# Optimization experiments

Hardware: AMD Instinct MI355X
Metric: run time of the kernel (lower is better)

Reference implementation:

```python
import math
import jax, jax.numpy as jnp
import numpy as np

TAU = 2.0
THR = 1.0
ALPHA = 10.0

T, B, IN_DIM, OUT_DIM = 64, 128, 2048, 2048


def setup_inputs() -> dict:
    key = jax.random.key(0)
    k1, k2, k3 = jax.random.split(key, 3)
    x_seq = jax.random.normal(k1, (T, B, IN_DIM), dtype=jnp.float32)
    # scale like nn.Linear default init so membrane potentials are O(1)
    W = jax.random.normal(k2, (OUT_DIM, IN_DIM), dtype=jnp.float32) / math.sqrt(IN_DIM)
    b = jax.random.normal(k3, (OUT_DIM,), dtype=jnp.float32) * 0.01
    return {"x_seq": x_seq, "W": W, "b": b}


def spike(x):
    # forward: hard threshold (surrogate gradient only matters in bwd)
    return (x > 0).astype(x.dtype)


def reference(x_seq, W, b):
    decay = math.exp(-1.0 / TAU)
    # hoist the linear layer out of the recurrence: one big GEMM
    cur_seq = jnp.einsum("tbi,oi->tbo", x_seq, W) + b  # (T, B, OUT_DIM)
    mem0 = jnp.zeros((x_seq.shape[1], W.shape[0]), dtype=x_seq.dtype)

    def step(mem, cur):
        mem = mem * decay + cur
        spk = spike(mem - THR)
        mem = mem - spk * THR
        return mem, spk

    _, spk_seq = jax.lax.scan(step, mem0, cur_seq)
    return spk_seq  # (T, B, OUT_DIM)
```

## Files before the change

kernel.cpp:

```cpp
#include <hip/hip_runtime.h>
#include <hip/hip_bf16.h>
#include <math.h>


typedef unsigned short u16;
typedef __attribute__((ext_vector_type(8))) short bf16x8;
typedef __attribute__((ext_vector_type(4))) float f32x4;

constexpr int T_STEPS = 64;
constexpr int BATCH   = 128;
constexpr int K_DIM   = 2048;
constexpr int N_DIM   = 2048;
constexpr int M_DIM   = T_STEPS * BATCH;
constexpr int NCHAIN  = BATCH * N_DIM;

constexpr float DECAY_F32 = (float)0.6065306597126334;
constexpr float BAND      = 2e-4f;

__global__ __launch_bounds__(512, 2)
void gemm_bf16x3f(const float* __restrict__ X, const float* __restrict__ W,
                  const float* __restrict__ bias, float* __restrict__ C,
                  unsigned int* __restrict__ counters) {
    extern __shared__ __align__(16) u16 smem[];
    u16* const sAh = smem;
    u16* const sAl = smem + 2 * 8192;
    u16* const sBh = smem + 4 * 8192;
    u16* const sBl = smem + 4 * 8192 + 2 * 4096;

    const int tid  = threadIdx.x;
    const int orig = blockIdx.x + gridDim.x * blockIdx.y;
    if (orig == 0 && tid < 128) counters[tid] = 0u;

    const int wg   = (orig & 7) * 64 + (orig >> 3);
    const int m0   = (wg >> 4) * 256;
    const int n0   = (wg & 15) * 128;
    const int lane = tid & 63;
    const int wave = tid >> 6;
    const int wm   = wave >> 1;
    const int wn   = wave & 1;

    const int row_e = (tid >> 6) * 16 + (tid & 15);
    const int ks_e  = ((tid >> 4) & 3) * 8;
    const size_t a0f = (size_t)(m0 + row_e) * K_DIM + ks_e;
    const size_t a1f = (size_t)(m0 + 128 + row_e) * K_DIM + ks_e;
    const size_t b0f = (size_t)(n0 + row_e) * K_DIM + ks_e;
    const int wA0 = tid * 8;
    const int wA1 = 4096 + tid * 8;
    const int wB0 = tid * 8;

    f32x4 acc[4][4];
#pragma unroll
    for (int i = 0; i < 4; i++)
#pragma unroll
        for (int j = 0; j < 4; j++) acc[i][j] = (f32x4){0.f, 0.f, 0.f, 0.f};

    float4 g0[6], g1[6];

#define GLOAD(SET, kc) do {                                                  \
        const size_t k_ = (size_t)(kc) * 32;                                 \
        g##SET[0] = *(const float4*)(X + a0f + k_);                          \
        g##SET[1] = *(const float4*)(X + a0f + k_ + 4);                      \
        g##SET[2] = *(const float4*)(X + a1f + k_);                          \
        g##SET[3] = *(const float4*)(X + a1f + k_ + 4);                      \
        g##SET[4] = *(const float4*)(W + b0f + k_);                          \
        g##SET[5] = *(const float4*)(W + b0f + k_ + 4);                      \
    } while (0)

#define DEK8(v0, v1, HI, LO) do {                                            \
        const float f_[8] = {v0.x, v0.y, v0.z, v0.w, v1.x, v1.y, v1.z, v1.w};\
        unsigned int hp_[4], lp_[4];                                         \
        _Pragma("unroll")                                                    \
        for (int q_ = 0; q_ < 8; q_ += 2) {                                  \
            u16 hh_[2], ll_[2];                                              \
            _Pragma("unroll")                                                \
            for (int e_ = 0; e_ < 2; e_++) {                                 \
                __hip_bfloat16 hb_ = __float2bfloat16(f_[q_ + e_]);          \
                const float hf_ = __bfloat162float(hb_);                     \
                __hip_bfloat16 lb_ = __float2bfloat16(f_[q_ + e_] - hf_);    \
                hh_[e_] = *(u16*)&hb_;                                       \
                ll_[e_] = *(u16*)&lb_;                                       \
            }                                                                \
            hp_[q_ >> 1] = (unsigned int)hh_[0] | ((unsigned int)hh_[1] << 16); \
            lp_[q_ >> 1] = (unsigned int)ll_[0] | ((unsigned int)ll_[1] << 16); \
        }                                                                    \
        HI = make_uint4(hp_[0], hp_[1], hp_[2], hp_[3]);                     \
        LO = make_uint4(lp_[0], lp_[1], lp_[2], lp_[3]);                     \
    } while (0)

#define CONVWRITE(s, SET) do {                                               \
        uint4 hA0_, lA0_, hA1_, lA1_, hB_, lB_;                              \
        DEK8(g##SET[0], g##SET[1], hA0_, lA0_);                              \
        DEK8(g##SET[2], g##SET[3], hA1_, lA1_);                              \
        DEK8(g##SET[4], g##SET[5], hB_, lB_);                                \
        *(uint4*)&sAh[(s) * 8192 + wA0] = hA0_;                              \
        *(uint4*)&sAl[(s) * 8192 + wA0] = lA0_;                              \
        *(uint4*)&sAh[(s) * 8192 + wA1] = hA1_;                              \
        *(uint4*)&sAl[(s) * 8192 + wA1] = lA1_;                              \
        *(uint4*)&sBh[(s) * 4096 + wB0] = hB_;                               \
        *(uint4*)&sBl[(s) * 4096 + wB0] = lB_;                               \
    } while (0)

#define COMPUTE(rs) do {                                                     \
        bf16x8 fah[4], fal[4], fbh[4], fbl[4];                               \
        _Pragma("unroll")                                                    \
        for (int ti = 0; ti < 4; ti++) {                                     \
            const int ta = wm * 4 + ti;                                      \
            fah[ti] = *(const bf16x8*)&sAh[(rs) * 8192 + (ta * 64 + lane) * 8]; \
            fal[ti] = *(const bf16x8*)&sAl[(rs) * 8192 + (ta * 64 + lane) * 8]; \
        }                                                                    \
        _Pragma("unroll")                                                    \
        for (int tj = 0; tj < 4; tj++) {                                     \
            const int tb = wn * 4 + tj;                                      \
            fbh[tj] = *(const bf16x8*)&sBh[(rs) * 4096 + (tb * 64 + lane) * 8]; \
            fbl[tj] = *(const bf16x8*)&sBl[(rs) * 4096 + (tb * 64 + lane) * 8]; \
        }                                                                    \
        __builtin_amdgcn_s_setprio(1);                                       \
        _Pragma("unroll")                                                    \
        for (int ti = 0; ti < 4; ti++)                                       \
        _Pragma("unroll")                                                    \
        for (int tj = 0; tj < 4; tj++) {                                     \
            acc[ti][tj] = __builtin_amdgcn_mfma_f32_16x16x32_bf16(           \
                fah[ti], fbh[tj], acc[ti][tj], 0, 0, 0);                     \
            acc[ti][tj] = __builtin_amdgcn_mfma_f32_16x16x32_bf16(           \
                fah[ti], fbl[tj], acc[ti][tj], 0, 0, 0);                     \
            acc[ti][tj] = __builtin_amdgcn_mfma_f32_16x16x32_bf16(           \
                fal[ti], fbh[tj], acc[ti][tj], 0, 0, 0);                     \
        }                                                                    \
        __builtin_amdgcn_s_setprio(0);                                       \
    } while (0)

#define BAR do {                                                             \
        __builtin_amdgcn_sched_barrier(0);                                   \
        __builtin_amdgcn_s_barrier();                                        \
        __builtin_amdgcn_sched_barrier(0);                                   \
    } while (0)
#define VMW(n) do {                                                          \
        asm volatile("s_waitcnt vmcnt(" #n ")" ::: "memory");                \
        __builtin_amdgcn_sched_barrier(0);                                   \
    } while (0)
#define LGKM0 do {                                                           \
        asm volatile("s_waitcnt lgkmcnt(0)" ::: "memory");                   \
        __builtin_amdgcn_sched_barrier(0);                                   \
    } while (0)

    GLOAD(0, 0);
    VMW(0);
    CONVWRITE(0, 0);
    GLOAD(1, 1);
    LGKM0;

    for (int kc = 0; kc < 60; kc += 2) {
        BAR;
        GLOAD(0, kc + 2);
        VMW(6);
        CONVWRITE(1, 1);
        LGKM0;
        COMPUTE(0);
        BAR;
        GLOAD(1, kc + 3);
        VMW(6);
        CONVWRITE(0, 0);
        LGKM0;
        COMPUTE(1);
    }
    BAR;
    GLOAD(0, 62);
    VMW(6);
    CONVWRITE(1, 1);
    LGKM0;
    COMPUTE(0);
    BAR;
    GLOAD(1, 63);
    VMW(6);
    CONVWRITE(0, 0);
    LGKM0;
    COMPUTE(1);
    BAR;
    VMW(0);
    CONVWRITE(1, 1);
    LGKM0;
    COMPUTE(0);
    BAR;
    COMPUTE(1);

#undef LGKM0
#undef VMW
#undef BAR
#undef COMPUTE
#undef CONVWRITE
#undef DEK8
#undef GLOAD

#pragma unroll
    for (int tj = 0; tj < 4; tj++) {
        const int n  = n0 + wn * 64 + tj * 16 + (lane & 15);
        const float bv = bias[n];
#pragma unroll
        for (int ti = 0; ti < 4; ti++) {
            const int mbase = m0 + wm * 64 + ti * 16 + (lane >> 4) * 4;
#pragma unroll
            for (int r = 0; r < 4; r++)
                C[(size_t)(mbase + r) * N_DIM + n] = acc[ti][tj][r] + bv;
        }
    }
}

__global__ __launch_bounds__(256)
void lif_scan_band2(float* __restrict__ buf, unsigned int* __restrict__ counters,
                    unsigned int* __restrict__ worklist) {
    const int idx = (blockIdx.x * 256 + threadIdx.x) * 2;
    float mem[2]  = {0.f, 0.f};
    bool  flag[2] = {false, false};
#pragma unroll
    for (int t = 0; t < T_STEPS; t++) {
        const size_t off = (size_t)t * NCHAIN + idx;
        const float2 v = *(const float2*)(buf + off);
        const float c[2] = {v.x, v.y};
        float s[2];
#pragma unroll
        for (int q = 0; q < 2; q++) {
            mem[q] = __fadd_rn(__fmul_rn(mem[q], DECAY_F32), c[q]);
            const float d = __fsub_rn(mem[q], 1.0f);
            const bool spk = d > 0.0f;
            if (fabsf(d) < BAND) flag[q] = true;
            s[q] = spk ? 1.0f : 0.0f;
            if (spk) mem[q] = __fsub_rn(mem[q], 1.0f);
        }
        *(float2*)(buf + off) = make_float2(s[0], s[1]);
    }
    const int b = idx >> 11;
#pragma unroll
    for (int q = 0; q < 2; q++) {
        if (flag[q]) {
            const unsigned int p = atomicAdd(&counters[b], 1u);
            worklist[b * 2048 + p] = (unsigned int)((idx + q) & 2047);
        }
    }
}

#define RG 16
#define RJ 4
#define BKR 64

__global__ __launch_bounds__(256)
void lif_repair2(const float* __restrict__ X, const float* __restrict__ W,
                 const float* __restrict__ bias,
                 const unsigned int* __restrict__ counters,
                 const unsigned int* __restrict__ worklist,
                 float* __restrict__ out) {
    __shared__ float sX[BKR][T_STEPS + 1];
    __shared__ float sW[RG][BKR + 1];
    __shared__ float scur[T_STEPS][RG + 1];
    __shared__ float sspk[T_STEPS][RG + 1];
    __shared__ int   so[RG];

    const int b = blockIdx.x / RJ;
    const int j = blockIdx.x % RJ;
    const unsigned int n_b = counters[b];
    if (n_b == 0) return;
    const int ngroups = (int)(n_b + RG - 1) / RG;

    const int tid = threadIdx.x;
    const int t   = tid & 63;
    const int oi  = tid >> 6;

    const int ts  = tid >> 2;
    const int kq  = (tid & 3) * 16;
    const int wo  = tid >> 4;
    const int wkq = (tid & 15) * 4;

    for (int g = j; g < ngroups; g += RJ) {
        if (tid < RG) {
            const int slot = g * RG + tid;
            so[tid] = (slot < (int)n_b) ? (int)worklist[b * 2048 + slot] : -1;
        }
        __syncthreads();

        float Csum[4] = {0.f, 0.f, 0.f, 0.f};
        float P[4]    = {0.f, 0.f, 0.f, 0.f};

        float4 rx[4];
        float4 rw;
        {
            const float* srcx = &X[(size_t)(ts * BATCH + b) * K_DIM + kq];
#pragma unroll
            for (int q = 0; q < 4; q++) rx[q] = *(const float4*)(srcx + q * 4);
            const int o = so[wo];
            rw = (o >= 0) ? *(const float4*)&W[(size_t)o * K_DIM + wkq]
                          : make_float4(0.f, 0.f, 0.f, 0.f);
        }

        for (int c = 0; c < K_DIM / BKR; c++) {
            if (c > 0 && (c % 5) == 0) {
#pragma unroll
                for (int q = 0; q < 4; q++) {
                    Csum[q] = __fadd_rn(Csum[q], P[q]);
                    P[q] = 0.f;
                }
            }
            __syncthreads();
#pragma unroll
            for (int q = 0; q < 4; q++) {
                sX[kq + q * 4 + 0][ts] = rx[q].x;
                sX[kq + q * 4 + 1][ts] = rx[q].y;
                sX[kq + q * 4 + 2][ts] = rx[q].z;
                sX[kq + q * 4 + 3][ts] = rx[q].w;
            }
            sW[wo][wkq + 0] = rw.x; sW[wo][wkq + 1] = rw.y;
            sW[wo][wkq + 2] = rw.z; sW[wo][wkq + 3] = rw.w;
            if (c + 1 < K_DIM / BKR) {
                const int k1 = (c + 1) * BKR;
                const float* srcx = &X[(size_t)(ts * BATCH + b) * K_DIM + k1 + kq];
#pragma unroll
                for (int q = 0; q < 4; q++) rx[q] = *(const float4*)(srcx + q * 4);
                const int o = so[wo];
                rw = (o >= 0) ? *(const float4*)&W[(size_t)o * K_DIM + k1 + wkq]
                              : make_float4(0.f, 0.f, 0.f, 0.f);
            }
            __syncthreads();
#pragma unroll 8
            for (int k = 0; k < BKR; k++) {
                const float xv = sX[k][t];
#pragma unroll
                for (int q = 0; q < 4; q++)
                    P[q] = fmaf(xv, sW[oi * 4 + q][k], P[q]);
            }
        }
        __syncthreads();
#pragma unroll
        for (int q = 0; q < 4; q++) {
            Csum[q] = __fadd_rn(Csum[q], P[q]);
            const int o = so[oi * 4 + q];
            scur[t][oi * 4 + q] = (o >= 0) ? __fadd_rn(Csum[q], bias[o]) : 0.f;
        }
        __syncthreads();
        if (tid < RG && so[tid] >= 0) {
            float mem = 0.0f;
            for (int tt = 0; tt < T_STEPS; tt++) {
                mem = __fadd_rn(__fmul_rn(mem, DECAY_F32), scur[tt][tid]);
                const float d = __fsub_rn(mem, 1.0f);
                const bool spk = d > 0.0f;
                sspk[tt][tid] = spk ? 1.0f : 0.0f;
                if (spk) mem = __fsub_rn(mem, 1.0f);
            }
        }
        __syncthreads();
#pragma unroll
        for (int q = 0; q < 4; q++) {
            const int o = so[oi * 4 + q];
            if (o >= 0)
                out[(size_t)t * NCHAIN + (size_t)b * N_DIM + o] = sspk[t][oi * 4 + q];
        }
        __syncthreads();
    }
}

__global__ __launch_bounds__(256)
void lif_openblas_q320(const float* __restrict__ X, const float* __restrict__ W,
                       const float* __restrict__ bias, float* __restrict__ out) {
    __shared__ float As[16][T_STEPS + 4];
    __shared__ float Ws[16][64 + 4];
    __shared__ float curbuf[T_STEPS][64 + 1];
    const int tid = threadIdx.x;
    const int o0 = blockIdx.x * 64, b0 = blockIdx.y;
    const int tm = (tid & 15) * 4, tn = (tid >> 4) * 4;
    float Csum[4][4], Pacc[4][4];
#pragma unroll
    for (int i = 0; i < 4; i++)
#pragma unroll
        for (int j = 0; j < 4; j++) { Csum[i][j] = 0.f; Pacc[i][j] = 0.f; }
    for (int c = 0; c < K_DIM / 16; c++) {
        if (c > 0 && (c % 20) == 0) {
#pragma unroll
            for (int i = 0; i < 4; i++)
#pragma unroll
                for (int j = 0; j < 4; j++) {
                    Csum[i][j] = __fadd_rn(Csum[i][j], Pacc[i][j]);
                    Pacc[i][j] = 0.f;
                }
        }
        const int k0 = c * 16;
        {
            const int t = tid >> 2, kq = (tid & 3) * 4;
            const float4 av = *(const float4*)&X[(size_t)(t * BATCH + b0) * K_DIM + k0 + kq];
            As[kq + 0][t] = av.x; As[kq + 1][t] = av.y;
            As[kq + 2][t] = av.z; As[kq + 3][t] = av.w;
            const float4 wv = *(const float4*)&W[(size_t)(o0 + t) * K_DIM + k0 + kq];
            Ws[kq + 0][t] = wv.x; Ws[kq + 1][t] = wv.y;
            Ws[kq + 2][t] = wv.z; Ws[kq + 3][t] = wv.w;
        }
        __syncthreads();
#pragma unroll
        for (int k = 0; k < 16; k++) {
            float a[4], w[4];
#pragma unroll
            for (int i = 0; i < 4; i++) a[i] = As[k][tm + i];
#pragma unroll
            for (int j = 0; j < 4; j++) w[j] = Ws[k][tn + j];
#pragma unroll
            for (int i = 0; i < 4; i++)
#pragma unroll
                for (int j = 0; j < 4; j++) Pacc[i][j] = fmaf(a[i], w[j], Pacc[i][j]);
        }
        __syncthreads();
    }
#pragma unroll
    for (int i = 0; i < 4; i++)
#pragma unroll
        for (int j = 0; j < 4; j++)
            curbuf[tm + i][tn + j] =
                __fadd_rn(__fadd_rn(Csum[i][j], Pacc[i][j]), bias[o0 + tn + j]);
    __syncthreads();
    if (tid < 64) {
        float mem = 0.0f;
#pragma unroll
        for (int t = 0; t < T_STEPS; t++) {
            mem = __fadd_rn(__fmul_rn(mem, DECAY_F32), curbuf[t][tid]);
            const float d = __fsub_rn(mem, 1.0f);
            const bool spk = d > 0.0f;
            out[(size_t)t * NCHAIN + (size_t)b0 * N_DIM + o0 + tid] = spk ? 1.0f : 0.0f;
            if (spk) mem = __fsub_rn(mem, 1.0f);
        }
    }
}

extern "C" void kernel_launch(void* const* d_in, const int* in_sizes, int n_in,
                              void* d_out, int out_size, void* d_ws, size_t ws_size,
                              hipStream_t stream) {
    const float* x = nullptr; const float* W = nullptr; const float* bias = nullptr;
    for (int i = 0; i < n_in; i++) {
        if      (in_sizes[i] == M_DIM * K_DIM) x    = (const float*)d_in[i];
        else if (in_sizes[i] == N_DIM * K_DIM) W    = (const float*)d_in[i];
        else if (in_sizes[i] == N_DIM)         bias = (const float*)d_in[i];
    }
    if (!x)    x    = (const float*)d_in[0];
    if (!W)    W    = (const float*)d_in[1];
    if (!bias) bias = (const float*)d_in[2];
    float* out = (float*)d_out;

    const size_t off_cnt = 0;
    const size_t off_wl  = 512;
    const size_t need    = off_wl + (size_t)128 * 2048 * 4;

    if (ws_size < need) {
        dim3 grid(N_DIM / 64, BATCH);
        lif_openblas_q320<<<grid, 256, 0, stream>>>(x, W, bias, out);
        return;
    }

    char* ws = (char*)d_ws;
    unsigned int* counters = (unsigned int*)(ws + off_cnt);
    unsigned int* worklist = (unsigned int*)(ws + off_wl);

    dim3 ggrid(N_DIM / 128, M_DIM / 256);
    gemm_bf16x3f<<<ggrid, 512, 98304, stream>>>(x, W, bias, out, counters);
    lif_scan_band2<<<NCHAIN / 512, 256, 0, stream>>>(out, counters, worklist);
    lif_repair2<<<128 * RJ, 256, 0, stream>>>(x, W, bias, counters, worklist, out);
}
```

Before: 432.6 us.

## Fuse LIF scan into GEMM epilogue via timestep-major M tiling and LDS

The GEMM M-tile is regrouped so each workgroup covers all 64 timesteps for 4 batch rows and 128 output columns. The biased currents are staged in LDS, and the LIF recurrence, spike output and near-threshold worklist append run in the GEMM epilogue. This removes the separate scan kernel and the full round trip of the current tensor through global memory. In exchange, dynamic LDS grows, a 64-step serial scan is added to the end of each GEMM block, A-row loads become strided gathers of 4-row groups, and the counter reset moves to a hipMemsetAsync.

```diff
diff --git a/kernel.cpp b/kernel.cpp
--- a/kernel.cpp
+++ b/kernel.cpp
@@ -18,9 +18,10 @@
 constexpr float BAND      = 2e-4f;
 
 __global__ __launch_bounds__(512, 2)
-void gemm_bf16x3f(const float* __restrict__ X, const float* __restrict__ W,
-                  const float* __restrict__ bias, float* __restrict__ C,
-                  unsigned int* __restrict__ counters) {
+void gemm_lif(const float* __restrict__ X, const float* __restrict__ W,
+              const float* __restrict__ bias, float* __restrict__ out,
+              unsigned int* __restrict__ counters,
+              unsigned int* __restrict__ worklist) {
     extern __shared__ __align__(16) u16 smem[];
     u16* const sAh = smem;
     u16* const sAl = smem + 2 * 8192;
@@ -29,21 +30,19 @@
 
     const int tid  = threadIdx.x;
     const int orig = blockIdx.x + gridDim.x * blockIdx.y;
-    if (orig == 0 && tid < 128) counters[tid] = 0u;
-
     const int wg   = (orig & 7) * 64 + (orig >> 3);
-    const int m0   = (wg >> 4) * 256;
+    const int b0i  = (wg >> 4) * 4;
     const int n0   = (wg & 15) * 128;
     const int lane = tid & 63;
     const int wave = tid >> 6;
     const int wm   = wave >> 1;
     const int wn   = wave & 1;
 
-    const int row_e = (tid >> 6) * 16 + (tid & 15);
-    const int ks_e  = ((tid >> 4) & 3) * 8;
-    const size_t a0f = (size_t)(m0 + row_e) * K_DIM + ks_e;
-    const size_t a1f = (size_t)(m0 + 128 + row_e) * K_DIM + ks_e;
-    const size_t b0f = (size_t)(n0 + row_e) * K_DIM + ks_e;
+    const int re   = (tid >> 6) * 16 + (tid & 15);
+    const int ks_e = ((tid >> 4) & 3) * 8;
+    const size_t a0f = (size_t)((re >> 2) * 128 + b0i + (re & 3)) * K_DIM + ks_e;
+    const size_t a1f = (size_t)(((re >> 2) + 32) * 128 + b0i + (re & 3)) * K_DIM + ks_e;
+    const size_t b0f = (size_t)(n0 + re) * K_DIM + ks_e;
     const int wA0 = tid * 8;
     const int wA1 = 4096 + tid * 8;
     const int wB0 = tid * 8;
@@ -191,49 +190,43 @@
 #undef DEK8
 #undef GLOAD
 
+    __syncthreads();
+    float* const curL = (float*)smem;
+
 #pragma unroll
     for (int tj = 0; tj < 4; tj++) {
-        const int n  = n0 + wn * 64 + tj * 16 + (lane & 15);
-        const float bv = bias[n];
+        const int col = wn * 64 + tj * 16 + (lane & 15);
+        const float bv = bias[n0 + col];
 #pragma unroll
         for (int ti = 0; ti < 4; ti++) {
-            const int mbase = m0 + wm * 64 + ti * 16 + (lane >> 4) * 4;
+            const int rb = wm * 64 + ti * 16 + (lane >> 4) * 4;
 #pragma unroll
             for (int r = 0; r < 4; r++)
-                C[(size_t)(mbase + r) * N_DIM + n] = acc[ti][tj][r] + bv;
-        }
-    }
-}
-
-__global__ __launch_bounds__(256)
-void lif_scan_band2(float* __restrict__ buf, unsigned int* __restrict__ counters,
-                    unsigned int* __restrict__ worklist) {
-    const int idx = (blockIdx.x * 256 + threadIdx.x) * 2;
-    float mem[2]  = {0.f, 0.f};
-    bool  flag[2] = {false, false};
-#pragma unroll
-    for (int t = 0; t < T_STEPS; t++) {
-        const size_t off = (size_t)t * NCHAIN + idx;
-        const float2 v = *(const float2*)(buf + off);
-        const float c[2] = {v.x, v.y};
-        float s[2];
-#pragma unroll
-        for (int q = 0; q < 2; q++) {
-            mem[q] = __fadd_rn(__fmul_rn(mem[q], DECAY_F32), c[q]);
-            const float d = __fsub_rn(mem[q], 1.0f);
+                curL[(rb + r) * 129 + col] = acc[ti][tj][r] + bv;
+        }
+    }
+    __syncthreads();
+
+    {
+        const int bl  = tid >> 7;
+        const int col = tid & 127;
+        const int b   = b0i + bl;
+        const int o   = n0 + col;
+        float mem = 0.0f;
+        bool flag = false;
+#pragma unroll
+        for (int t = 0; t < T_STEPS; t++) {
+            const float cv = curL[(t * 4 + bl) * 129 + col];
+            mem = __fadd_rn(__fmul_rn(mem, DECAY_F32), cv);
+            const float d = __fsub_rn(mem, 1.0f);
             const bool spk = d > 0.0f;
-            if (fabsf(d) < BAND) flag[q] = true;
-            s[q] = spk ? 1.0f : 0.0f;
-            if (spk) mem[q] = __fsub_rn(mem[q], 1.0f);
-        }
-        *(float2*)(buf + off) = make_float2(s[0], s[1]);
-    }
-    const int b = idx >> 11;
-#pragma unroll
-    for (int q = 0; q < 2; q++) {
-        if (flag[q]) {
+            if (fabsf(d) < BAND) flag = true;
+            out[(size_t)t * NCHAIN + (size_t)b * N_DIM + o] = spk ? 1.0f : 0.0f;
+            if (spk) mem = __fsub_rn(mem, 1.0f);
+        }
+        if (flag) {
             const unsigned int p = atomicAdd(&counters[b], 1u);
-            worklist[b * 2048 + p] = (unsigned int)((idx + q) & 2047);
+            worklist[b * 2048 + p] = (unsigned int)o;
         }
     }
 }
@@ -452,8 +445,9 @@
     unsigned int* counters = (unsigned int*)(ws + off_cnt);
     unsigned int* worklist = (unsigned int*)(ws + off_wl);
 
+    hipMemsetAsync(counters, 0, 512, stream);
+
     dim3 ggrid(N_DIM / 128, M_DIM / 256);
-    gemm_bf16x3f<<<ggrid, 512, 98304, stream>>>(x, W, bias, out, counters);
-    lif_scan_band2<<<NCHAIN / 512, 256, 0, stream>>>(out, counters, worklist);
+    gemm_lif<<<ggrid, 512, 132096, stream>>>(x, W, bias, out, counters, worklist);
     lif_repair2<<<128 * RJ, 256, 0, stream>>>(x, W, bias, counters, worklist, out);
 }
```

Measured after the change: 417.7 us, median of 2. -3.5%, faster.
